# Kernel optimization log

Hardware: AMD Instinct MI355X
Metric: run time of the kernel (lower is better)

## Reference

```python
import jax, jax.numpy as jnp
import numpy as np

TAU = 2.0          # gumbel-softmax temperature (module default)
NUM_GROUPS = 2
NUM_VARS = 320
EPS = 1e-7


def setup_inputs() -> dict:
    key = jax.random.key(0)
    k1, k2, k3, k4 = jax.random.split(key, 4)
    B, S, D = 32, 2048, 512
    GK = NUM_GROUPS * NUM_VARS            # 640
    dpg = 256 // NUM_GROUPS               # codevector_dim // num_groups = 128
    hidden_states = jax.random.normal(k1, (B, S, D), dtype=jnp.float32)
    mask_time_indices = jnp.ones((B, S), dtype=bool)
    gumbel_noise = jax.random.gumbel(k2, (B * S * NUM_GROUPS, NUM_VARS), dtype=jnp.float32)
    W = jax.random.normal(k3, (GK, D), dtype=jnp.float32) * (1.0 / np.sqrt(D))
    b = jnp.zeros((GK,), dtype=jnp.float32)
    codevectors = jax.random.uniform(k4, (1, GK, dpg), dtype=jnp.float32)
    return {"hidden_states": hidden_states, "mask_time_indices": mask_time_indices,
            "gumbel_noise": gumbel_noise, "W": W, "b": b, "codevectors": codevectors}


def reference(hidden_states, mask_time_indices, gumbel_noise, W, b, codevectors):
    B, S, D = hidden_states.shape
    G, K = NUM_GROUPS, NUM_VARS
    N = B * S

    # linear projection to logits: (B,S,G*K)
    logits = jnp.einsum('bsd,kd->bsk', hidden_states, W) + b
    logits_flat = logits.reshape(N * G, K)

    # training path: gumbel-softmax with hard straight-through
    y_soft = jax.nn.softmax((logits_flat + gumbel_noise) / TAU, axis=-1)
    idx = jnp.argmax(y_soft, axis=-1)
    y_hard = jax.nn.one_hot(idx, K, dtype=y_soft.dtype)
    probs = y_hard + y_soft - jax.lax.stop_gradient(y_soft)   # (N*G, K)

    # perplexity over the plain (no-gumbel) softmax distribution
    soft_dist = jax.nn.softmax(logits_flat.reshape(N, G, K), axis=-1)
    m = mask_time_indices.reshape(-1)[:, None, None]
    marginal = jnp.where(m, soft_dist, 0.0).sum(axis=0) / mask_time_indices.sum()   # (G, K)
    perplexity = jnp.exp(-jnp.sum(marginal * jnp.log(marginal + EPS), axis=-1)).sum()

    # weighted sum of codevectors per group (avoids (N, G*K, d) intermediate)
    cv = codevectors.reshape(G, K, -1)                         # (G, K, d/G)
    out = jnp.einsum('ngk,gkd->ngd', probs.reshape(N, G, K), cv).reshape(B, S, -1)
    return out, perplexity
```

## Files before the change

### kernel.cpp

```cpp
#include <hip/hip_runtime.h>


#define GG   2
#define KK   320
#define NN   65536
#define DD   512
#define DPG  128
#define EPSL 1e-7f
#define NCPY 8
#define BUFB 24576

typedef __attribute__((ext_vector_type(8))) short bf16x8;
typedef __attribute__((ext_vector_type(4))) float f32x4;
typedef __attribute__((address_space(1))) void glb_void;
typedef __attribute__((address_space(3))) void lds_void;

static __device__ __forceinline__ unsigned short f2bf_rne(float f) {
    unsigned u = __float_as_uint(f);
    u += 0x7FFFu + ((u >> 16) & 1u);
    return (unsigned short)(u >> 16);
}

static __device__ __forceinline__ bf16x8 pack8_rne(float4 v0, float4 v1) {
    union { unsigned short s[8]; bf16x8 b; } u;
    u.s[0] = f2bf_rne(v0.x); u.s[1] = f2bf_rne(v0.y);
    u.s[2] = f2bf_rne(v0.z); u.s[3] = f2bf_rne(v0.w);
    u.s[4] = f2bf_rne(v1.x); u.s[5] = f2bf_rne(v1.y);
    u.s[6] = f2bf_rne(v1.z); u.s[7] = f2bf_rne(v1.w);
    return u.b;
}

static __device__ __forceinline__ unsigned ordf(float f) {
    unsigned u = __float_as_uint(f);
    return (u & 0x80000000u) ? ~u : (u | 0x80000000u);
}

__global__ __launch_bounds__(256) void prep_all(
    const float* __restrict__ H, short* __restrict__ Hbf,
    const float* __restrict__ W, short* __restrict__ Wf,
    float* __restrict__ marg, const int* __restrict__ mask,
    float* __restrict__ cnt_out, int* __restrict__ done)
{
    const int b = blockIdx.x, tid = threadIdx.x;
    if (b < 16384) {
        const size_t base = ((size_t)b * 256 + tid) * 8;
        float4 v0 = *(const float4*)(H + base);
        float4 v1 = *(const float4*)(H + base + 4);
        *(bf16x8*)(Hbf + base) = pack8_rne(v0, v1);
    } else if (b < 16544) {
        int gt = (b - 16384) * 256 + tid;
        int w  = gt >> 6, l = gt & 63;
        int col = 16 * (w >> 4) + (l & 15);
        int k0  = 32 * (w & 15) + 8 * (l >> 4);
        const float* src = W + (size_t)col * DD + k0;
        float4 v0 = *(const float4*)(src);
        float4 v1 = *(const float4*)(src + 4);
        *(bf16x8*)(Wf + (size_t)w * 512 + (size_t)l * 8) = pack8_rne(v0, v1);
    } else {
        __shared__ float red[256];
        for (int i = tid; i < NCPY * GG * KK; i += 256) marg[i] = 0.f;
        if (tid == 0) *done = 0;
        const int4* m4 = (const int4*)mask;
        int c = 0;
#pragma unroll 4
        for (int i = tid; i < NN / 4; i += 256) {
            int4 v = m4[i];
            c += (v.x != 0) + (v.y != 0) + (v.z != 0) + (v.w != 0);
        }
        red[tid] = (float)c;
        __syncthreads();
        for (int s = 128; s > 0; s >>= 1) {
            if (tid < s) red[tid] += red[tid + s];
            __syncthreads();
        }
        if (tid == 0) *cnt_out = red[0];
    }
}

__global__ __launch_bounds__(512, 4) void vq_main(
    const short* Hbf, const int* __restrict__ mask,
    const float* __restrict__ gumbel, const short* __restrict__ Wf,
    const float* __restrict__ bias, const float* __restrict__ cv,
    int* __restrict__ idxW, float* marg,
    int fused, float* __restrict__ out,
    const float* __restrict__ cnt_in, int* done, float* __restrict__ perp_out)
{
    __shared__ __align__(16) char smem[2 * BUFB];
    __shared__ float    red_s[256];
    __shared__ unsigned red_k[256];
    __shared__ float    wrowS[64];
    __shared__ int      idxf[64];
    __shared__ int      lastflag;

    const int tid = threadIdx.x;
    const int l   = tid & 63, wid = tid >> 6;
    const int rh  = wid >> 2, hc = wid & 3;
    const int g   = blockIdx.x & 1;
    const int T   = blockIdx.x >> 1;
    const int n0  = T * 64;
    const int q   = l >> 4,  ln = l & 15;

    const short* gsrc0[3];
    int stepB[3];
#pragma unroll
    for (int j = 0; j < 3; ++j) {
        const int k = wid * 3 + j;
        if (k < 4) {
            gsrc0[j] = Hbf + (size_t)(n0 + 16 * k + (l & 15)) * 512 + 8 * (l >> 4);
            stepB[j] = 64;
        } else {
            gsrc0[j] = Wf + (size_t)((g * 20 + (k - 4)) * 16) * 512 + (size_t)l * 8;
            stepB[j] = 1024;
        }
    }

#define ISSUE(t_, b_)                                                          \
    { _Pragma("unroll")                                                        \
      for (int j = 0; j < 3; ++j) {                                            \
          const int k = wid * 3 + j;                                           \
          const short* gsrc = (const short*)((const char*)gsrc0[j] + (t_) * stepB[j]); \
          char* ldst = smem + (b_)*BUFB + k * 1024;                            \
          __builtin_amdgcn_global_load_lds((const glb_void*)gsrc, (lds_void*)ldst, 16, 0, 0); \
      } }

    f32x4 acc[2][5];
    const f32x4 vzero = {0.f, 0.f, 0.f, 0.f};
#pragma unroll
    for (int a = 0; a < 2; ++a)
#pragma unroll
        for (int b = 0; b < 5; ++b) acc[a][b] = vzero;

#define COMPUTE(b_)                                                            \
    { const char* bb_ = smem + (b_)*BUFB;                                      \
      bf16x8 Ar[2], Br[5];                                                     \
      _Pragma("unroll")                                                        \
      for (int rf = 0; rf < 2; ++rf)                                           \
          Ar[rf] = *(const bf16x8*)(bb_ + (rh * 2 + rf) * 1024 + l * 16);      \
      _Pragma("unroll")                                                        \
      for (int cf = 0; cf < 5; ++cf)                                           \
          Br[cf] = *(const bf16x8*)(bb_ + 4096 + (hc * 5 + cf) * 1024 + l * 16); \
      __builtin_amdgcn_s_setprio(1);                                           \
      _Pragma("unroll")                                                        \
      for (int cf = 0; cf < 5; ++cf) {                                         \
          acc[0][cf] = __builtin_amdgcn_mfma_f32_16x16x32_bf16(Ar[0], Br[cf], acc[0][cf], 0, 0, 0); \
          acc[1][cf] = __builtin_amdgcn_mfma_f32_16x16x32_bf16(Ar[1], Br[cf], acc[1][cf], 0, 0, 0); } \
      __builtin_amdgcn_s_setprio(0); }

    ISSUE(0, 0)
#pragma unroll 1
    for (int c = 0; c < 16; ++c) {
        asm volatile("s_waitcnt vmcnt(0)" ::: "memory");
        __builtin_amdgcn_sched_barrier(0);
        __builtin_amdgcn_s_barrier();
        if (c + 1 < 16) ISSUE(c + 1, (c + 1) & 1)
        __builtin_amdgcn_sched_barrier(0);
        COMPUTE(c & 1)
    }

    float bb[5];
#pragma unroll
    for (int cf = 0; cf < 5; ++cf) bb[cf] = bias[g * KK + hc * 80 + 16 * cf + ln];

    float gum[8][5];
#pragma unroll
    for (int rf = 0; rf < 2; ++rf)
#pragma unroll
        for (int reg = 0; reg < 4; ++reg) {
            const int row = 32 * rh + 16 * rf + 4 * q + reg;
            const float* gp = gumbel + ((size_t)(n0 + row) * GG + g) * KK + hc * 80 + ln;
#pragma unroll
            for (int cf = 0; cf < 5; ++cf) gum[rf * 4 + reg][cf] = gp[16 * cf];
        }
    __builtin_amdgcn_sched_barrier(0);

#pragma unroll
    for (int cf = 0; cf < 5; ++cf)
#pragma unroll
        for (int rf = 0; rf < 2; ++rf) {
            acc[rf][cf][0] += bb[cf]; acc[rf][cf][1] += bb[cf];
            acc[rf][cf][2] += bb[cf]; acc[rf][cf][3] += bb[cf];
        }

#pragma unroll
    for (int rf = 0; rf < 2; ++rf) {
#pragma unroll
        for (int reg = 0; reg < 4; ++reg) {
            const int row = 32 * rh + 16 * rf + 4 * q + reg;
            float s = 0.f, zm = -3.0e38f;
            int zi = 0;
#pragma unroll
            for (int cf = 0; cf < 5; ++cf) {
                float v = acc[rf][cf][reg];
                float z = v + gum[rf * 4 + reg][cf];
                if (z > zm) { zm = z; zi = hc * 80 + 16 * cf + ln; }
                float e = __expf(v);
                s += e;
                acc[rf][cf][reg] = e;
            }
            unsigned key = (ordf(zm) & 0xFFFFFE00u) | (unsigned)(511 - zi);
#pragma unroll
            for (int d = 1; d <= 8; d <<= 1) {
                s += __shfl_xor(s, d);
                unsigned ko = (unsigned)__shfl_xor((int)key, d);
                key = key > ko ? key : ko;
            }
            if (ln == 0) {
                const int base = row * 4 + hc;
                red_s[base] = s;
                red_k[base] = key;
            }
        }
    }
    __syncthreads();

    if (tid < 64) {
        const int b0 = tid * 4;
        float Z = red_s[b0] + red_s[b0 + 1] + red_s[b0 + 2] + red_s[b0 + 3];
        unsigned km = red_k[b0];
        km = km > red_k[b0 + 1] ? km : red_k[b0 + 1];
        km = km > red_k[b0 + 2] ? km : red_k[b0 + 2];
        km = km > red_k[b0 + 3] ? km : red_k[b0 + 3];
        const int ib = 511 - (int)(km & 511u);
        idxf[tid]  = ib;
        if (!fused) idxW[(size_t)(n0 + tid) * GG + g] = ib;
        wrowS[tid] = ((mask[n0 + tid] != 0) ? 1.0f : 0.0f) / Z;
    }
    __syncthreads();

    float cs[5] = {0.f, 0.f, 0.f, 0.f, 0.f};
#pragma unroll
    for (int rf = 0; rf < 2; ++rf) {
#pragma unroll
        for (int reg = 0; reg < 4; ++reg) {
            const int row = 32 * rh + 16 * rf + 4 * q + reg;
            const float wv = wrowS[row];
#pragma unroll
            for (int cf = 0; cf < 5; ++cf)
                cs[cf] += acc[rf][cf][reg] * wv;
        }
    }
    {
        float* mc = marg + (size_t)(blockIdx.x & (NCPY - 1)) * (GG * KK);
#pragma unroll
        for (int cf = 0; cf < 5; ++cf) {
            float v = cs[cf];
            v += __shfl_xor(v, 16);
            v += __shfl_xor(v, 32);
            if (l < 16) atomicAdd(&mc[g * KK + hc * 80 + 16 * cf + l], v);
        }
    }

    if (fused) {
#pragma unroll
        for (int i = 0; i < 4; ++i) {
            const int e = tid + 512 * i;
            const int row = e >> 5, d4 = e & 31;
            const float4 v = ((const float4*)cv)[((size_t)g * KK + idxf[row]) * 32 + d4];
            ((float4*)(out + (size_t)(n0 + row) * 256 + g * DPG))[d4] = v;
        }
    }

    asm volatile("s_waitcnt vmcnt(0)" ::: "memory");
    __syncthreads();
    if (tid == 0) {
        int old = atomicAdd(done, 1);
        lastflag = (old == 2047) ? 1 : 0;
    }
    __syncthreads();
    if (lastflag) {
        const float invc = 1.0f / cnt_in[0];
        float hg[GG];
#pragma unroll
        for (int gg = 0; gg < GG; ++gg) {
            float h = 0.f;
            for (int c = tid; c < KK; c += 512) {
                float m = 0.f;
#pragma unroll
                for (int x = 0; x < NCPY; ++x)
                    m += atomicAdd(&marg[x * (GG * KK) + gg * KK + c], 0.0f);
                m *= invc;
                h += m * logf(m + EPSL);
            }
#pragma unroll
            for (int d = 1; d < 64; d <<= 1) h += __shfl_xor(h, d);
            if (l == 0) red_s[wid] = h;
            __syncthreads();
            if (tid == 0) {
                float t = 0.f;
                for (int wv = 0; wv < 8; ++wv) t += red_s[wv];
                red_s[64 + gg] = t;
            }
            __syncthreads();
            hg[gg] = red_s[64 + gg];
        }
        if (tid == 0) perp_out[0] = expf(-hg[0]) + expf(-hg[1]);
    }
}

__global__ __launch_bounds__(256) void gather_kernel(
    const int* __restrict__ idxW, const float* __restrict__ cv,
    float* __restrict__ out)
{
    const int e = blockIdx.x * 256 + threadIdx.x;
    const int n = e >> 6, s4 = e & 63, g = s4 >> 5, d4 = s4 & 31;
    const int idx = idxW[(size_t)n * GG + g];
    const float4 v = ((const float4*)cv)[((size_t)g * KK + idx) * 32 + d4];
    ((float4*)out)[e] = v;
}

extern "C" void kernel_launch(void* const* d_in, const int* in_sizes, int n_in,
                              void* d_out, int out_size, void* d_ws, size_t ws_size,
                              hipStream_t stream)
{
    const float* H      = (const float*)d_in[0];
    const int*   mask   = (const int*)d_in[1];
    const float* gumbel = (const float*)d_in[2];
    const float* W      = (const float*)d_in[3];
    const float* bias   = (const float*)d_in[4];
    const float* cv     = (const float*)d_in[5];

    float*  out  = (float*)d_out;
    float*  marg = (float*)d_ws;
    float*  cnt  = (float*)((char*)d_ws + 24576);
    int*    done = (int*)((char*)d_ws + 24580);
    short*  Wf   = (short*)((char*)d_ws + 32768);
    int*    idxW = (int*)((char*)d_ws + 32768 + 655360);

    const size_t hbf_off  = 2 * 1024 * 1024;
    const size_t hbf_need = hbf_off + (size_t)64 * 1024 * 1024;
    const int fused = (ws_size >= hbf_need) ? 1 : 0;
    short* Hbf = fused ? (short*)((char*)d_ws + hbf_off) : (short*)d_out;

    prep_all<<<16545, 256, 0, stream>>>(H, Hbf, W, Wf, marg, mask, cnt, done);
    vq_main<<<2048, 512, 0, stream>>>(Hbf, mask, gumbel, Wf, bias, cv, idxW, marg,
                                      fused, out, cnt, done,
                                      out + (size_t)NN * GG * DPG);
    if (!fused)
        gather_kernel<<<16384, 256, 0, stream>>>(idxW, cv, out);
}
```

Before: 136.6 us.

## Fuse fp32-to-bf16 conversion of hidden states into main GEMM kernel with triple buffering

```diff
diff --git a/kernel.cpp b/kernel.cpp
--- a/kernel.cpp
+++ b/kernel.cpp
@@ -11,6 +11,7 @@
 #define BUFB 24576
 
 typedef __attribute__((ext_vector_type(8))) short bf16x8;
+typedef __attribute__((ext_vector_type(4))) short bf16x4;
 typedef __attribute__((ext_vector_type(4))) float f32x4;
 typedef __attribute__((address_space(1))) void glb_void;
 typedef __attribute__((address_space(3))) void lds_void;
@@ -30,25 +31,26 @@
     return u.b;
 }
 
+static __device__ __forceinline__ bf16x4 pack4_rne(float4 v) {
+    union { unsigned short s[4]; bf16x4 b; } u;
+    u.s[0] = f2bf_rne(v.x); u.s[1] = f2bf_rne(v.y);
+    u.s[2] = f2bf_rne(v.z); u.s[3] = f2bf_rne(v.w);
+    return u.b;
+}
+
 static __device__ __forceinline__ unsigned ordf(float f) {
     unsigned u = __float_as_uint(f);
     return (u & 0x80000000u) ? ~u : (u | 0x80000000u);
 }
 
 __global__ __launch_bounds__(256) void prep_all(
-    const float* __restrict__ H, short* __restrict__ Hbf,
     const float* __restrict__ W, short* __restrict__ Wf,
     float* __restrict__ marg, const int* __restrict__ mask,
     float* __restrict__ cnt_out, int* __restrict__ done)
 {
     const int b = blockIdx.x, tid = threadIdx.x;
-    if (b < 16384) {
-        const size_t base = ((size_t)b * 256 + tid) * 8;
-        float4 v0 = *(const float4*)(H + base);
-        float4 v1 = *(const float4*)(H + base + 4);
-        *(bf16x8*)(Hbf + base) = pack8_rne(v0, v1);
-    } else if (b < 16544) {
-        int gt = (b - 16384) * 256 + tid;
+    if (b < 160) {
+        int gt = b * 256 + tid;
         int w  = gt >> 6, l = gt & 63;
         int col = 16 * (w >> 4) + (l & 15);
         int k0  = 32 * (w & 15) + 8 * (l >> 4);
@@ -78,14 +80,13 @@
 }
 
 __global__ __launch_bounds__(512, 4) void vq_main(
-    const short* Hbf, const int* __restrict__ mask,
+    const float* __restrict__ Hf, const int* __restrict__ mask,
     const float* __restrict__ gumbel, const short* __restrict__ Wf,
     const float* __restrict__ bias, const float* __restrict__ cv,
-    int* __restrict__ idxW, float* marg,
-    int fused, float* __restrict__ out,
+    float* marg, float* __restrict__ out,
     const float* __restrict__ cnt_in, int* done, float* __restrict__ perp_out)
 {
-    __shared__ __align__(16) char smem[2 * BUFB];
+    __shared__ __align__(16) char smem[3 * BUFB];
     __shared__ float    red_s[256];
     __shared__ unsigned red_k[256];
     __shared__ float    wrowS[64];
@@ -100,28 +101,30 @@
     const int n0  = T * 64;
     const int q   = l >> 4,  ln = l & 15;
 
-    const short* gsrc0[3];
-    int stepB[3];
+    const short* gsrcB[3];
 #pragma unroll
     for (int j = 0; j < 3; ++j) {
-        const int k = wid * 3 + j;
-        if (k < 4) {
-            gsrc0[j] = Hbf + (size_t)(n0 + 16 * k + (l & 15)) * 512 + 8 * (l >> 4);
-            stepB[j] = 64;
-        } else {
-            gsrc0[j] = Wf + (size_t)((g * 20 + (k - 4)) * 16) * 512 + (size_t)l * 8;
-            stepB[j] = 1024;
-        }
-    }
-
-#define ISSUE(t_, b_)                                                          \
+        const int bidx = wid + 8 * j;
+        gsrcB[j] = Wf + (size_t)((g * 20 + (bidx < 20 ? bidx : 0)) * 16) * 512 + (size_t)l * 8;
+    }
+
+#define ISSUE_B(t_, b_)                                                        \
     { _Pragma("unroll")                                                        \
       for (int j = 0; j < 3; ++j) {                                            \
-          const int k = wid * 3 + j;                                           \
-          const short* gsrc = (const short*)((const char*)gsrc0[j] + (t_) * stepB[j]); \
-          char* ldst = smem + (b_)*BUFB + k * 1024;                            \
-          __builtin_amdgcn_global_load_lds((const glb_void*)gsrc, (lds_void*)ldst, 16, 0, 0); \
+          const int bidx = wid + 8 * j;                                        \
+          if (bidx < 20) {                                                     \
+              const short* gsrc = (const short*)((const char*)gsrcB[j] + ((t_) << 10)); \
+              char* ldst = smem + (b_)*BUFB + (4 + bidx) * 1024;               \
+              __builtin_amdgcn_global_load_lds((const glb_void*)gsrc, (lds_void*)ldst, 16, 0, 0); \
+          }                                                                    \
       } }
+
+    const int arow = tid >> 3, aseg = tid & 7;
+    const float* Asrc0 = Hf + (size_t)(n0 + arow) * DD + 4 * aseg;
+    const int aoff = (arow >> 4) * 1024 + (((arow & 15) | ((aseg >> 1) << 4)) * 16) + (aseg & 1) * 8;
+
+#define A_LOAD(t_)  (*(const float4*)(Asrc0 + 32 * (t_)))
+#define A_WRITE(v_, b_)  { *(bf16x4*)(smem + (b_)*BUFB + aoff) = pack4_rne(v_); }
 
     f32x4 acc[2][5];
     const f32x4 vzero = {0.f, 0.f, 0.f, 0.f};
@@ -146,15 +149,29 @@
           acc[1][cf] = __builtin_amdgcn_mfma_f32_16x16x32_bf16(Ar[1], Br[cf], acc[1][cf], 0, 0, 0); } \
       __builtin_amdgcn_s_setprio(0); }
 
-    ISSUE(0, 0)
+    ISSUE_B(0, 0)
+    {
+        float4 av0 = A_LOAD(0);
+        ISSUE_B(1, 1)
+        A_WRITE(av0, 0)
+    }
+
 #pragma unroll 1
     for (int c = 0; c < 16; ++c) {
-        asm volatile("s_waitcnt vmcnt(0)" ::: "memory");
+        if (c + 1 < 16) {
+            if (wid < 4) asm volatile("s_waitcnt vmcnt(3) lgkmcnt(0)" ::: "memory");
+            else         asm volatile("s_waitcnt vmcnt(2) lgkmcnt(0)" ::: "memory");
+        } else {
+            asm volatile("s_waitcnt vmcnt(0) lgkmcnt(0)" ::: "memory");
+        }
         __builtin_amdgcn_sched_barrier(0);
         __builtin_amdgcn_s_barrier();
-        if (c + 1 < 16) ISSUE(c + 1, (c + 1) & 1)
+        float4 av;
+        if (c + 1 < 16) av = A_LOAD(c + 1);
+        if (c + 2 < 16) ISSUE_B(c + 2, (c + 2) % 3)
         __builtin_amdgcn_sched_barrier(0);
-        COMPUTE(c & 1)
+        COMPUTE(c % 3)
+        if (c + 1 < 16) A_WRITE(av, (c + 1) % 3)
     }
 
     float bb[5];
@@ -222,7 +239,6 @@
         km = km > red_k[b0 + 3] ? km : red_k[b0 + 3];
         const int ib = 511 - (int)(km & 511u);
         idxf[tid]  = ib;
-        if (!fused) idxW[(size_t)(n0 + tid) * GG + g] = ib;
         wrowS[tid] = ((mask[n0 + tid] != 0) ? 1.0f : 0.0f) / Z;
     }
     __syncthreads();
@@ -250,14 +266,12 @@
         }
     }
 
-    if (fused) {
-#pragma unroll
-        for (int i = 0; i < 4; ++i) {
-            const int e = tid + 512 * i;
-            const int row = e >> 5, d4 = e & 31;
-            const float4 v = ((const float4*)cv)[((size_t)g * KK + idxf[row]) * 32 + d4];
-            ((float4*)(out + (size_t)(n0 + row) * 256 + g * DPG))[d4] = v;
-        }
+#pragma unroll
+    for (int i = 0; i < 4; ++i) {
+        const int e = tid + 512 * i;
+        const int row = e >> 5, d4 = e & 31;
+        const float4 v = ((const float4*)cv)[((size_t)g * KK + idxf[row]) * 32 + d4];
+        ((float4*)(out + (size_t)(n0 + row) * 256 + g * DPG))[d4] = v;
     }
 
     asm volatile("s_waitcnt vmcnt(0)" ::: "memory");
@@ -295,17 +309,6 @@
         }
         if (tid == 0) perp_out[0] = expf(-hg[0]) + expf(-hg[1]);
     }
-}
-
-__global__ __launch_bounds__(256) void gather_kernel(
-    const int* __restrict__ idxW, const float* __restrict__ cv,
-    float* __restrict__ out)
-{
-    const int e = blockIdx.x * 256 + threadIdx.x;
-    const int n = e >> 6, s4 = e & 63, g = s4 >> 5, d4 = s4 & 31;
-    const int idx = idxW[(size_t)n * GG + g];
-    const float4 v = ((const float4*)cv)[((size_t)g * KK + idx) * 32 + d4];
-    ((float4*)out)[e] = v;
 }
 
 extern "C" void kernel_launch(void* const* d_in, const int* in_sizes, int n_in,
@@ -324,17 +327,8 @@
     float*  cnt  = (float*)((char*)d_ws + 24576);
     int*    done = (int*)((char*)d_ws + 24580);
     short*  Wf   = (short*)((char*)d_ws + 32768);
-    int*    idxW = (int*)((char*)d_ws + 32768 + 655360);
-
-    const size_t hbf_off  = 2 * 1024 * 1024;
-    const size_t hbf_need = hbf_off + (size_t)64 * 1024 * 1024;
-    const int fused = (ws_size >= hbf_need) ? 1 : 0;
-    short* Hbf = fused ? (short*)((char*)d_ws + hbf_off) : (short*)d_out;
-
-    prep_all<<<16545, 256, 0, stream>>>(H, Hbf, W, Wf, marg, mask, cnt, done);
-    vq_main<<<2048, 512, 0, stream>>>(Hbf, mask, gumbel, Wf, bias, cv, idxW, marg,
-                                      fused, out, cnt, done,
-                                      out + (size_t)NN * GG * DPG);
-    if (!fused)
-        gather_kernel<<<16384, 256, 0, stream>>>(idxW, cv, out);
-}
+
+    prep_all<<<161, 256, 0, stream>>>(W, Wf, marg, mask, cnt, done);
+    vq_main<<<2048, 512, 0, stream>>>(H, mask, gumbel, Wf, bias, cv, marg, out,
+                                      cnt, done, out + (size_t)NN * GG * DPG);
+}
```

Result: no change. 137.8 us (+0.8%).
